# Kernel tuning notes

Hardware: AMD Instinct MI355X
Metric: run time of the kernel (lower is better)

Reference implementation:

```python
import jax, jax.numpy as jnp
import numpy as np

D_MODEL = 1024
N_HEADS = 16
MAX_SEQ_LEN = 2048

def setup_inputs() -> dict:
    key = jax.random.key(0)
    ks = jax.random.split(key, 4)
    B, L, D = 2, 2048, D_MODEL
    s = 0.02
    x = jax.random.normal(ks[0], (B, L, D), dtype=jnp.float32)
    qkv_w = jax.random.normal(ks[1], (D, 3 * D), dtype=jnp.float32) * s
    qkv_b = jnp.zeros((3 * D,), dtype=jnp.float32)
    proj_w = jax.random.normal(ks[2], (D, D), dtype=jnp.float32) * s
    proj_b = jnp.zeros((D,), dtype=jnp.float32)
    bias_table = jax.random.normal(ks[3], (2 * MAX_SEQ_LEN - 1, N_HEADS), dtype=jnp.float32) * s
    return {"x": x, "qkv_w": qkv_w, "qkv_b": qkv_b, "proj_w": proj_w, "proj_b": proj_b, "bias_table": bias_table}

def reference(x, qkv_w, qkv_b, proj_w, proj_b, bias_table):
    B, L, D = x.shape
    H = N_HEADS
    dk = D // H
    scale = dk ** -0.5
    # fused qkv projection: (B,L,3,H,dk)
    qkv = (x @ qkv_w + qkv_b).reshape(B, L, 3, H, dk)
    q = qkv[:, :, 0].transpose(0, 2, 1, 3)  # (B,H,L,dk)
    k = qkv[:, :, 1].transpose(0, 2, 1, 3)
    v = qkv[:, :, 2].transpose(0, 2, 1, 3)
    attn = jnp.einsum("bhqd,bhkd->bhqk", q, k) * scale  # (B,H,L,L)
    # relative position bias gather (Swin-style)
    coords = jnp.arange(L)
    rel_idx = coords[None, :] - coords[:, None] + (MAX_SEQ_LEN - 1)  # (L,L)
    rel_bias = bias_table[rel_idx]  # (L,L,H)
    attn = attn + rel_bias.transpose(2, 0, 1)[None]  # (B,H,L,L)
    attn = jax.nn.softmax(attn, axis=-1)
    out = jnp.einsum("bhqk,bhkd->bhqd", attn, v)  # (B,H,L,dk)
    out = out.transpose(0, 2, 1, 3).reshape(B, L, D)
    return out @ proj_w + proj_b
```

## Files before the change

### kernel.cpp

```cpp
#include <hip/hip_runtime.h>
#include <stdint.h>

typedef __attribute__((ext_vector_type(4))) float    f32x4;
typedef f32x4 __attribute__((aligned(4)))   f32x4u;
typedef __attribute__((ext_vector_type(8))) short    bf16x8;
typedef __attribute__((ext_vector_type(2))) uint32_t u32x2;
typedef __attribute__((ext_vector_type(4))) uint32_t u32x4;

#define MFMA16(a,b,c) __builtin_amdgcn_mfma_f32_16x16x32_bf16((a),(b),(c),0,0,0)

__device__ __forceinline__ uint16_t f2bf(float f){
  uint32_t u = __float_as_uint(f);
  return (uint16_t)((u + 0x7FFFu + ((u >> 16) & 1u)) >> 16);
}

__device__ __forceinline__ uint32_t pk_bf16(float lo, float hi){
  uint32_t r; asm("v_cvt_pk_bf16_f32 %0, %1, %2" : "=v"(r) : "v"(lo), "v"(hi)); return r;
}

__device__ __forceinline__ float fast_exp2(float x){
  float r; asm("v_exp_f32 %0, %1" : "=v"(r) : "v"(x)); return r;
}
__device__ __forceinline__ float fast_log2(float x){
  float r; asm("v_log_f32 %0, %1" : "=v"(r) : "v"(x)); return r;
}

__device__ __forceinline__ float bfl(uint32_t u){ return __uint_as_float(u << 16); }
__device__ __forceinline__ float bfh(uint32_t u){ return __uint_as_float(u & 0xffff0000u); }

__device__ __forceinline__ void gload16(const uint16_t* g, uint16_t* l){
  __builtin_amdgcn_global_load_lds((const __attribute__((address_space(1))) uint32_t*)g,
                                   (__attribute__((address_space(3))) uint32_t*)l, 16, 0, 0);
}

__global__ void k_cvt(const float* __restrict__ in, uint16_t* __restrict__ out){
  const size_t i = (size_t)(blockIdx.x*256 + threadIdx.x) * 4;
  const f32x4 v = *(const f32x4*)(in + i);
  u32x2 pk = {pk_bf16(v[0], v[1]), pk_bf16(v[2], v[3])};
  *(u32x2*)(out + i) = pk;
}

__global__ void k_tcvt(const float* __restrict__ in, uint16_t* __restrict__ out, int K, int N){
  __shared__ float tile[64][65];
  const int k0 = blockIdx.y*64, n0 = blockIdx.x*64;
  const int tc = threadIdx.x & 63, tr = threadIdx.x >> 6;
  #pragma unroll
  for (int p=0;p<16;p++){ int r = p*4 + tr; tile[r][tc] = in[(size_t)(k0+r)*N + n0 + tc]; }
  __syncthreads();
  #pragma unroll
  for (int p=0;p<16;p++){ int r = p*4 + tr; out[(size_t)(n0+r)*K + k0 + tc] = f2bf(tile[tc][r]); }
}

__global__ void k_biast(const float* __restrict__ in, float* __restrict__ out){
  const int i = blockIdx.x*256 + threadIdx.x;
  if (i < 4095*16) out[(i & 15)*4096 + (i >> 4)] = in[i] * 1.4426950408889634f;
}

template<int EPI>
__global__ __launch_bounds__(256, 2) void k_gemm(
    const uint16_t* __restrict__ A, const uint16_t* __restrict__ Bt,
    const float* __restrict__ bias,
    uint16_t* __restrict__ qo, uint16_t* __restrict__ ko, uint16_t* __restrict__ vto,
    float* __restrict__ outf)
{
  __shared__ __align__(16) uint16_t at[128*64];
  __shared__ __align__(16) uint16_t bt[128*64];
  const int tid = threadIdx.x;
  const int lane = tid & 63, w = tid >> 6;
  const int g = lane >> 4, li = lane & 15;
  const int wr = w >> 1, wc = w & 1;
  const int m0 = blockIdx.y * 128, n0 = blockIdx.x * 128;

  f32x4 acc[4][4] = {};

  const int srow = tid >> 3;
  const int scg  = (tid & 7) ^ (srow & 7);

  for (int kt_ = 0; kt_ < 16; kt_++){
    const int kk = kt_*64;
    __syncthreads();
    #pragma unroll
    for (int j = 0; j < 4; j++){
      gload16(A  + (size_t)(m0 + j*32 + srow)*1024 + kk + scg*8, at + (j*256+tid)*8);
      gload16(Bt + (size_t)(n0 + j*32 + srow)*1024 + kk + scg*8, bt + (j*256+tid)*8);
    }
    asm volatile("s_waitcnt vmcnt(0)" ::: "memory");
    __syncthreads();

    bf16x8 af[2][4], bfr[2][4];
    #pragma unroll
    for (int mi=0; mi<4; mi++){
      int row = wr*64 + mi*16 + li, sw = row & 7;
      af[0][mi] = *(const bf16x8*)(at + row*64 + ((g     ^ sw)*8));
      af[1][mi] = *(const bf16x8*)(at + row*64 + (((4+g) ^ sw)*8));
    }
    #pragma unroll
    for (int ni=0; ni<4; ni++){
      int row = wc*64 + ni*16 + li, sw = row & 7;
      bfr[0][ni] = *(const bf16x8*)(bt + row*64 + ((g     ^ sw)*8));
      bfr[1][ni] = *(const bf16x8*)(bt + row*64 + (((4+g) ^ sw)*8));
    }
    #pragma unroll
    for (int s=0; s<2; s++)
      #pragma unroll
      for (int mi=0; mi<4; mi++)
        #pragma unroll
        for (int ni=0; ni<4; ni++)
          acc[mi][ni] = MFMA16(af[s][mi], bfr[s][ni], acc[mi][ni]);
  }

  if (EPI == 0){
    #pragma unroll
    for (int ni=0; ni<4; ni++){
      const int c = n0 + wc*64 + ni*16 + li;
      const float bv = bias[c];
      const int which = c >> 10, cc = c & 1023;
      const int h = cc >> 6, d = cc & 63;
      #pragma unroll
      for (int mi=0; mi<4; mi++){
        const int trow = m0 + wr*64 + mi*16 + g*4;
        const int b_ = trow >> 11, lcl = trow & 2047;
        const f32x4 v4 = acc[mi][ni];
        if (which == 0){
          uint16_t* dst = qo + (((size_t)(b_*16 + h)*2048 + lcl)*64 + d);
          #pragma unroll
          for (int r=0;r<4;r++) dst[(size_t)r*64] = f2bf((v4[r] + bv) * 0.18033688011112042f);
        } else if (which == 1){
          uint16_t* dst = ko + (((size_t)(b_*16 + h)*2048 + lcl)*64 + d);
          #pragma unroll
          for (int r=0;r<4;r++) dst[(size_t)r*64] = f2bf(v4[r] + bv);
        } else {
          u32x2 pk = {pk_bf16(v4[0]+bv, v4[1]+bv), pk_bf16(v4[2]+bv, v4[3]+bv)};
          *(u32x2*)(vto + (((size_t)(b_*16 + h)*64 + d)*2048 + lcl)) = pk;
        }
      }
    }
  } else {
    #pragma unroll
    for (int ni=0; ni<4; ni++){
      const int c = n0 + wc*64 + ni*16 + li;
      const float bv = bias[c];
      #pragma unroll
      for (int mi=0; mi<4; mi++){
        const int trow = m0 + wr*64 + mi*16 + g*4;
        float* dst = outf + (size_t)trow*1024 + c;
        const f32x4 v4 = acc[mi][ni];
        #pragma unroll
        for (int r=0;r<4;r++) dst[(size_t)r*1024] = v4[r] + bv;
      }
    }
  }
}

__device__ __forceinline__ void attn_tile(
    int t, bool last, int tid, int g, int li, int srow, int scg,
    const uint16_t* kbase, const uint16_t* vbase, const float* bb,
    const uint16_t* ktc, uint16_t* ktn, const uint16_t* vtc, uint16_t* vtn, uint16_t* pl,
    const bf16x8 (&qf)[2][2], bf16x8 ones,
    f32x4 (&o)[4][2], f32x4 (&o4)[2], float& mrun0, float& mrun1)
{
  const int kv0 = t*64;

  f32x4 bv[2][4];
  #pragma unroll
  for (int c=0;c<2;c++)
    #pragma unroll
    for (int mf=0;mf<4;mf++)
      bv[c][mf] = *(const f32x4u*)(bb + kv0 + mf*16 + g*4 - c*16 - li);
  asm volatile("" ::: "memory");

  if (!last){
    const int kv1 = kv0 + 64;
    gload16(kbase + (size_t)(kv1+srow)*64 + scg*8,         ktn + tid*8);
    gload16(kbase + (size_t)(kv1+srow+32)*64 + scg*8,      ktn + 2048 + tid*8);
    gload16(vbase + (size_t)srow*2048 + kv1 + scg*8,       vtn + tid*8);
    gload16(vbase + (size_t)(srow+32)*2048 + kv1 + scg*8,  vtn + 2048 + tid*8);
    asm volatile("s_waitcnt vmcnt(12)" ::: "memory");
  } else {
    asm volatile("s_waitcnt vmcnt(8)" ::: "memory");
  }
  __builtin_amdgcn_s_barrier();

  f32x4 sa[4][2];
  __builtin_amdgcn_s_setprio(1);
  #pragma unroll
  for (int mf=0; mf<4; mf++){
    const int row = mf*16 + li, sw = row & 7;
    bf16x8 a0 = *(const bf16x8*)(ktc + row*64 + ((g     ^ sw)*8));
    bf16x8 a1 = *(const bf16x8*)(ktc + row*64 + (((4+g) ^ sw)*8));
    #pragma unroll
    for (int c=0;c<2;c++){
      f32x4 cfr = {};
      cfr = MFMA16(a0, qf[c][0], cfr);
      cfr = MFMA16(a1, qf[c][1], cfr);
      sa[mf][c] = cfr;
    }
  }
  __builtin_amdgcn_s_setprio(0);

  float t0 = -__builtin_inff(), t1 = -__builtin_inff();
  #pragma unroll
  for (int mf=0; mf<4; mf++){
    sa[mf][0] += bv[0][mf];
    sa[mf][1] += bv[1][mf];
    #pragma unroll
    for (int r=0; r<4; r++){
      t0 = fmaxf(t0, sa[mf][0][r]);
      t1 = fmaxf(t1, sa[mf][1][r]);
    }
  }

  const int ok = (t0 <= mrun0 + 8.f) && (t1 <= mrun1 + 8.f);
  if (!__all(ok)){
    float r0 = t0, r1 = t1;
    r0 = fmaxf(r0, __shfl_xor(r0, 16)); r0 = fmaxf(r0, __shfl_xor(r0, 32));
    r1 = fmaxf(r1, __shfl_xor(r1, 16)); r1 = fmaxf(r1, __shfl_xor(r1, 32));
    const float mn0 = fmaxf(mrun0, r0), mn1 = fmaxf(mrun1, r1);
    const float a0 = fast_exp2(mrun0 - mn0), a1 = fast_exp2(mrun1 - mn1);
    #pragma unroll
    for (int mf=0; mf<4; mf++){ o[mf][0] *= a0; o[mf][1] *= a1; }
    o4[0] *= a0; o4[1] *= a1;
    mrun0 = mn0; mrun1 = mn1;
  }

  bf16x8 av[2][4];
  #pragma unroll
  for (int s=0; s<2; s++)
    #pragma unroll
    for (int mf=0; mf<4; mf++){
      const int row = mf*16 + li, sw = row & 7;
      av[s][mf] = *(const bf16x8*)(vtc + row*64 + (((4*s+g) ^ sw)*8));
    }

  const int swp2 = 2*(li & 7);
  #pragma unroll
  for (int c=0;c<2;c++){
    const float mr = c ? mrun1 : mrun0;
    #pragma unroll
    for (int mf=0; mf<4; mf++){
      float p0 = fast_exp2(sa[mf][c][0] - mr);
      float p1 = fast_exp2(sa[mf][c][1] - mr);
      float p2 = fast_exp2(sa[mf][c][2] - mr);
      float p3 = fast_exp2(sa[mf][c][3] - mr);
      u32x2 pk = {pk_bf16(p0,p1), pk_bf16(p2,p3)};
      *(u32x2*)(pl + li*64 + (((4*mf+g) ^ swp2)*4)) = pk;
    }
    __builtin_amdgcn_s_setprio(1);
    #pragma unroll
    for (int s=0; s<2; s++){
      bf16x8 pb = *(const bf16x8*)(pl + li*64 + (((8*s+2*g) ^ swp2)*4));
      o4[c] = MFMA16(ones, pb, o4[c]);
      #pragma unroll
      for (int mf=0; mf<4; mf++)
        o[mf][c] = MFMA16(av[s][mf], pb, o[mf][c]);
    }
    __builtin_amdgcn_s_setprio(0);
  }
  __builtin_amdgcn_s_barrier();
}

__global__ __launch_bounds__(256, 2) void k_attn(
    const uint16_t* __restrict__ qg, const uint16_t* __restrict__ kg,
    const uint16_t* __restrict__ vg, const float* __restrict__ biast,
    uint16_t* __restrict__ opart, float* __restrict__ spart)
{
  __shared__ __align__(16) uint16_t kt[2][64*64];
  __shared__ __align__(16) uint16_t vt[2][64*64];
  __shared__ __align__(16) uint16_t pt[4][16*64];
  const int tid = threadIdx.x;
  const int lane = tid & 63, w = tid >> 6;
  const int g = lane >> 4, li = lane & 15;
  const int bh = blockIdx.y, h = bh & 15, b_ = bh >> 4;
  const int id = blockIdx.x;
  const int split = id & 1, qxi = id >> 1;
  const int qw = qxi*128 + w*32;
  const int tg0 = split*16;

  bf16x8 qf[2][2];
  #pragma unroll
  for (int c=0;c<2;c++){
    const uint16_t* qp = qg + ((size_t)bh*2048 + qw + c*16 + li)*64 + g*8;
    qf[c][0] = *(const bf16x8*)(qp);
    qf[c][1] = *(const bf16x8*)(qp + 32);
  }
  bf16x8 ones = (bf16x8)(short)0;
  if (li == 0){ const short v = (short)0x3F80; ones = (bf16x8){v,v,v,v,v,v,v,v}; }

  f32x4 o[4][2] = {};
  f32x4 o4[2] = {};
  float mrun0 = -__builtin_inff(), mrun1 = -__builtin_inff();

  const uint16_t* kbase = kg + (size_t)bh*(2048*64);
  const uint16_t* vbase = vg + (size_t)bh*(64*2048);
  const int srow = tid >> 3;
  const int scg  = (tid & 7) ^ (srow & 7);
  const float* bb = biast + h*4096 + 2047 - qw;
  uint16_t* pl = &pt[w][0];

  const int kvp = tg0*64;
  gload16(kbase + (size_t)(kvp+srow)*64 + scg*8,        &kt[0][tid*8]);
  gload16(kbase + (size_t)(kvp+srow+32)*64 + scg*8,     &kt[0][2048 + tid*8]);
  gload16(vbase + (size_t)srow*2048 + kvp + scg*8,      &vt[0][tid*8]);
  gload16(vbase + (size_t)(srow+32)*2048 + kvp + scg*8, &vt[0][2048 + tid*8]);

  for (int tt = 0; tt < 16; tt += 2){
    attn_tile(tg0+tt,   false,      tid, g, li, srow, scg, kbase, vbase, bb,
              &kt[0][0], &kt[1][0], &vt[0][0], &vt[1][0], pl,
              qf, ones, o, o4, mrun0, mrun1);
    attn_tile(tg0+tt+1, tt == 14,   tid, g, li, srow, scg, kbase, vbase, bb,
              &kt[1][0], &kt[0][0], &vt[1][0], &vt[0][0], pl,
              qf, ones, o, o4, mrun0, mrun1);
  }

  const float ls0 = __shfl(o4[0][0], li);
  const float ls1 = __shfl(o4[1][0], li);
  const float inv0 = 1.0f / ls0, inv1 = 1.0f / ls1;
  const float sv0 = mrun0 + fast_log2(ls0);
  const float sv1 = mrun1 + fast_log2(ls1);
  #pragma unroll
  for (int c=0;c<2;c++){
    const float inv = c ? inv1 : inv0;
    const int token = b_*2048 + qw + c*16 + li;
    if (g == 0) spart[split*65536 + token*16 + h] = c ? sv1 : sv0;
    uint16_t* dst = opart + ((size_t)(split*4096 + token))*1024 + h*64;
    #pragma unroll
    for (int mf=0; mf<4; mf++){
      u32x2 pk = {pk_bf16(o[mf][c][0]*inv, o[mf][c][1]*inv),
                  pk_bf16(o[mf][c][2]*inv, o[mf][c][3]*inv)};
      *(u32x2*)(dst + mf*16 + g*4) = pk;
    }
  }
}

__global__ void k_merge(const uint16_t* __restrict__ op, const float* __restrict__ sp,
                        uint16_t* __restrict__ ao){
  const int gid = blockIdx.x*256 + threadIdx.x;
  const int token = gid >> 7, col0 = (gid & 127) * 8, h = col0 >> 6;
  const float s0 = sp[token*16 + h], s1 = sp[65536 + token*16 + h];
  const float sm = fmaxf(s0, s1);
  float w0 = fast_exp2(s0 - sm), w1 = fast_exp2(s1 - sm);
  const float inv = 1.0f / (w0 + w1);
  w0 *= inv; w1 *= inv;
  const size_t i0 = (size_t)token*1024 + col0;
  const u32x4 a = *(const u32x4*)(op + i0);
  const u32x4 b = *(const u32x4*)(op + (size_t)4096*1024 + i0);
  u32x4 r;
  #pragma unroll
  for (int j=0;j<4;j++){
    const float e0 = w0*bfl(a[j]) + w1*bfl(b[j]);
    const float e1 = w0*bfh(a[j]) + w1*bfh(b[j]);
    r[j] = pk_bf16(e0, e1);
  }
  *(u32x4*)(ao + i0) = r;
}

extern "C" void kernel_launch(void* const* d_in, const int* in_sizes, int n_in,
                              void* d_out, int out_size, void* d_ws, size_t ws_size,
                              hipStream_t stream)
{
  const float* x      = (const float*)d_in[0];
  const float* qkv_w  = (const float*)d_in[1];
  const float* qkv_b  = (const float*)d_in[2];
  const float* proj_w = (const float*)d_in[3];
  const float* proj_b = (const float*)d_in[4];
  const float* btab   = (const float*)d_in[5];
  float* out = (float*)d_out;

  char* p = (char*)d_ws;
  uint16_t* x_bf    = (uint16_t*)(p);
  uint16_t* qkv_wt  = (uint16_t*)(p + 8388608);
  uint16_t* proj_wt = (uint16_t*)(p + 14680064);
  uint16_t* q_buf   = (uint16_t*)(p + 16777216);
  uint16_t* k_buf   = (uint16_t*)(p + 25165824);
  uint16_t* vt_buf  = (uint16_t*)(p + 33554432);
  uint16_t* ao_buf  = (uint16_t*)(p + 41943040);
  float*    bias_t  = (float*)   (p + 50331648);

  uint16_t* o_part = (uint16_t*)d_out;
  float*    s_part = (float*)p;

  k_cvt  <<<dim3(4096),  dim3(256), 0, stream>>>(x, x_bf);
  k_tcvt <<<dim3(48,16), dim3(256), 0, stream>>>(qkv_w,  qkv_wt,  1024, 3072);
  k_tcvt <<<dim3(16,16), dim3(256), 0, stream>>>(proj_w, proj_wt, 1024, 1024);
  k_biast<<<dim3(256),   dim3(256), 0, stream>>>(btab, bias_t);

  k_gemm<0><<<dim3(24,32), dim3(256), 0, stream>>>(x_bf, qkv_wt, qkv_b, q_buf, k_buf, vt_buf, nullptr);
  k_attn   <<<dim3(32,32), dim3(256), 0, stream>>>(q_buf, k_buf, vt_buf, bias_t, o_part, s_part);
  k_merge  <<<dim3(2048),  dim3(256), 0, stream>>>(o_part, s_part, ao_buf);
  k_gemm<1><<<dim3(8,32),  dim3(256), 0, stream>>>(ao_buf, proj_wt, proj_b, nullptr, nullptr, nullptr, out);
}
```

Baseline: 131.0 us.

## Fuse bias-table prep into cvt kernel, narrow proj GEMM tile, dedupe bias loads

Merges the bias-table transpose into the x conversion kernel, removing one launch. Splits the output projection into its own GEMM with 128x64 tiles, doubling its grid from 256 to 512 blocks so more CUs are busy. In the attention tile, the 8 overlapping bias vector loads become 5 shared loads, and the vmcnt waits are adjusted to match. The trade-off is more blocks with less reuse per block in the projection GEMM.

```diff
diff --git a/kernel.cpp b/kernel.cpp
--- a/kernel.cpp
+++ b/kernel.cpp
@@ -33,11 +33,18 @@
                                    (__attribute__((address_space(3))) uint32_t*)l, 16, 0, 0);
 }
 
-__global__ void k_cvt(const float* __restrict__ in, uint16_t* __restrict__ out){
-  const size_t i = (size_t)(blockIdx.x*256 + threadIdx.x) * 4;
-  const f32x4 v = *(const f32x4*)(in + i);
-  u32x2 pk = {pk_bf16(v[0], v[1]), pk_bf16(v[2], v[3])};
-  *(u32x2*)(out + i) = pk;
+__global__ void k_cvtb(const float* __restrict__ in, uint16_t* __restrict__ out,
+                       const float* __restrict__ btab, float* __restrict__ bias_t){
+  const int bx = blockIdx.x;
+  if (bx < 4096){
+    const size_t i = (size_t)(bx*256 + threadIdx.x) * 4;
+    const f32x4 v = *(const f32x4*)(in + i);
+    u32x2 pk = {pk_bf16(v[0], v[1]), pk_bf16(v[2], v[3])};
+    *(u32x2*)(out + i) = pk;
+  } else {
+    const int i = (bx - 4096)*256 + threadIdx.x;
+    if (i < 4095*16) bias_t[(i & 15)*4096 + (i >> 4)] = btab[i] * 1.4426950408889634f;
+  }
 }
 
 __global__ void k_tcvt(const float* __restrict__ in, uint16_t* __restrict__ out, int K, int N){
@@ -51,17 +58,10 @@
   for (int p=0;p<16;p++){ int r = p*4 + tr; out[(size_t)(n0+r)*K + k0 + tc] = f2bf(tile[tc][r]); }
 }
 
-__global__ void k_biast(const float* __restrict__ in, float* __restrict__ out){
-  const int i = blockIdx.x*256 + threadIdx.x;
-  if (i < 4095*16) out[(i & 15)*4096 + (i >> 4)] = in[i] * 1.4426950408889634f;
-}
-
-template<int EPI>
 __global__ __launch_bounds__(256, 2) void k_gemm(
     const uint16_t* __restrict__ A, const uint16_t* __restrict__ Bt,
     const float* __restrict__ bias,
-    uint16_t* __restrict__ qo, uint16_t* __restrict__ ko, uint16_t* __restrict__ vto,
-    float* __restrict__ outf)
+    uint16_t* __restrict__ qo, uint16_t* __restrict__ ko, uint16_t* __restrict__ vto)
 {
   __shared__ __align__(16) uint16_t at[128*64];
   __shared__ __align__(16) uint16_t bt[128*64];
@@ -109,45 +109,94 @@
           acc[mi][ni] = MFMA16(af[s][mi], bfr[s][ni], acc[mi][ni]);
   }
 
-  if (EPI == 0){
-    #pragma unroll
-    for (int ni=0; ni<4; ni++){
-      const int c = n0 + wc*64 + ni*16 + li;
-      const float bv = bias[c];
-      const int which = c >> 10, cc = c & 1023;
-      const int h = cc >> 6, d = cc & 63;
+  #pragma unroll
+  for (int ni=0; ni<4; ni++){
+    const int c = n0 + wc*64 + ni*16 + li;
+    const float bv = bias[c];
+    const int which = c >> 10, cc = c & 1023;
+    const int h = cc >> 6, d = cc & 63;
+    #pragma unroll
+    for (int mi=0; mi<4; mi++){
+      const int trow = m0 + wr*64 + mi*16 + g*4;
+      const int b_ = trow >> 11, lcl = trow & 2047;
+      const f32x4 v4 = acc[mi][ni];
+      if (which == 0){
+        uint16_t* dst = qo + (((size_t)(b_*16 + h)*2048 + lcl)*64 + d);
+        #pragma unroll
+        for (int r=0;r<4;r++) dst[(size_t)r*64] = f2bf((v4[r] + bv) * 0.18033688011112042f);
+      } else if (which == 1){
+        uint16_t* dst = ko + (((size_t)(b_*16 + h)*2048 + lcl)*64 + d);
+        #pragma unroll
+        for (int r=0;r<4;r++) dst[(size_t)r*64] = f2bf(v4[r] + bv);
+      } else {
+        u32x2 pk = {pk_bf16(v4[0]+bv, v4[1]+bv), pk_bf16(v4[2]+bv, v4[3]+bv)};
+        *(u32x2*)(vto + (((size_t)(b_*16 + h)*64 + d)*2048 + lcl)) = pk;
+      }
+    }
+  }
+}
+
+__global__ __launch_bounds__(256, 2) void k_gemm2(
+    const uint16_t* __restrict__ A, const uint16_t* __restrict__ Bt,
+    const float* __restrict__ bias, float* __restrict__ outf)
+{
+  __shared__ __align__(16) uint16_t at[128*64];
+  __shared__ __align__(16) uint16_t bt[64*64];
+  const int tid = threadIdx.x;
+  const int lane = tid & 63, w = tid >> 6;
+  const int g = lane >> 4, li = lane & 15;
+  const int wr = w >> 1, wc = w & 1;
+  const int m0 = blockIdx.y * 128, n0 = blockIdx.x * 64;
+
+  f32x4 acc[4][2] = {};
+  const int srow = tid >> 3;
+  const int scg  = (tid & 7) ^ (srow & 7);
+
+  for (int kt_ = 0; kt_ < 16; kt_++){
+    const int kk = kt_*64;
+    __syncthreads();
+    #pragma unroll
+    for (int j = 0; j < 4; j++)
+      gload16(A  + (size_t)(m0 + j*32 + srow)*1024 + kk + scg*8, at + (j*256+tid)*8);
+    #pragma unroll
+    for (int j = 0; j < 2; j++)
+      gload16(Bt + (size_t)(n0 + j*32 + srow)*1024 + kk + scg*8, bt + (j*256+tid)*8);
+    asm volatile("s_waitcnt vmcnt(0)" ::: "memory");
+    __syncthreads();
+
+    bf16x8 af[2][4], bfr[2][2];
+    #pragma unroll
+    for (int mi=0; mi<4; mi++){
+      int row = wr*64 + mi*16 + li, sw = row & 7;
+      af[0][mi] = *(const bf16x8*)(at + row*64 + ((g     ^ sw)*8));
+      af[1][mi] = *(const bf16x8*)(at + row*64 + (((4+g) ^ sw)*8));
+    }
+    #pragma unroll
+    for (int ni=0; ni<2; ni++){
+      int row = wc*32 + ni*16 + li, sw = row & 7;
+      bfr[0][ni] = *(const bf16x8*)(bt + row*64 + ((g     ^ sw)*8));
+      bfr[1][ni] = *(const bf16x8*)(bt + row*64 + (((4+g) ^ sw)*8));
+    }
+    #pragma unroll
+    for (int s=0; s<2; s++)
       #pragma unroll
-      for (int mi=0; mi<4; mi++){
-        const int trow = m0 + wr*64 + mi*16 + g*4;
-        const int b_ = trow >> 11, lcl = trow & 2047;
-        const f32x4 v4 = acc[mi][ni];
-        if (which == 0){
-          uint16_t* dst = qo + (((size_t)(b_*16 + h)*2048 + lcl)*64 + d);
-          #pragma unroll
-          for (int r=0;r<4;r++) dst[(size_t)r*64] = f2bf((v4[r] + bv) * 0.18033688011112042f);
-        } else if (which == 1){
-          uint16_t* dst = ko + (((size_t)(b_*16 + h)*2048 + lcl)*64 + d);
-          #pragma unroll
-          for (int r=0;r<4;r++) dst[(size_t)r*64] = f2bf(v4[r] + bv);
-        } else {
-          u32x2 pk = {pk_bf16(v4[0]+bv, v4[1]+bv), pk_bf16(v4[2]+bv, v4[3]+bv)};
-          *(u32x2*)(vto + (((size_t)(b_*16 + h)*64 + d)*2048 + lcl)) = pk;
-        }
-      }
-    }
-  } else {
-    #pragma unroll
-    for (int ni=0; ni<4; ni++){
-      const int c = n0 + wc*64 + ni*16 + li;
-      const float bv = bias[c];
+      for (int mi=0; mi<4; mi++)
+        #pragma unroll
+        for (int ni=0; ni<2; ni++)
+          acc[mi][ni] = MFMA16(af[s][mi], bfr[s][ni], acc[mi][ni]);
+  }
+
+  #pragma unroll
+  for (int ni=0; ni<2; ni++){
+    const int c = n0 + wc*32 + ni*16 + li;
+    const float bv = bias[c];
+    #pragma unroll
+    for (int mi=0; mi<4; mi++){
+      const int trow = m0 + wr*64 + mi*16 + g*4;
+      float* dst = outf + (size_t)trow*1024 + c;
+      const f32x4 v4 = acc[mi][ni];
       #pragma unroll
-      for (int mi=0; mi<4; mi++){
-        const int trow = m0 + wr*64 + mi*16 + g*4;
-        float* dst = outf + (size_t)trow*1024 + c;
-        const f32x4 v4 = acc[mi][ni];
-        #pragma unroll
-        for (int r=0;r<4;r++) dst[(size_t)r*1024] = v4[r] + bv;
-      }
+      for (int r=0;r<4;r++) dst[(size_t)r*1024] = v4[r] + bv;
     }
   }
 }
@@ -161,12 +210,10 @@
 {
   const int kv0 = t*64;
 
-  f32x4 bv[2][4];
-  #pragma unroll
-  for (int c=0;c<2;c++)
-    #pragma unroll
-    for (int mf=0;mf<4;mf++)
-      bv[c][mf] = *(const f32x4u*)(bb + kv0 + mf*16 + g*4 - c*16 - li);
+  f32x4 bv5[5];
+  #pragma unroll
+  for (int j=0;j<5;j++)
+    bv5[j] = *(const f32x4u*)(bb + kv0 + (j-1)*16 + g*4 - li);
   asm volatile("" ::: "memory");
 
   if (!last){
@@ -175,9 +222,9 @@
     gload16(kbase + (size_t)(kv1+srow+32)*64 + scg*8,      ktn + 2048 + tid*8);
     gload16(vbase + (size_t)srow*2048 + kv1 + scg*8,       vtn + tid*8);
     gload16(vbase + (size_t)(srow+32)*2048 + kv1 + scg*8,  vtn + 2048 + tid*8);
-    asm volatile("s_waitcnt vmcnt(12)" ::: "memory");
+    asm volatile("s_waitcnt vmcnt(9)" ::: "memory");
   } else {
-    asm volatile("s_waitcnt vmcnt(8)" ::: "memory");
+    asm volatile("s_waitcnt vmcnt(5)" ::: "memory");
   }
   __builtin_amdgcn_s_barrier();
 
@@ -201,8 +248,8 @@
   float t0 = -__builtin_inff(), t1 = -__builtin_inff();
   #pragma unroll
   for (int mf=0; mf<4; mf++){
-    sa[mf][0] += bv[0][mf];
-    sa[mf][1] += bv[1][mf];
+    sa[mf][0] += bv5[mf+1];
+    sa[mf][1] += bv5[mf];
     #pragma unroll
     for (int r=0; r<4; r++){
       t0 = fmaxf(t0, sa[mf][0][r]);
@@ -379,13 +426,12 @@
   uint16_t* o_part = (uint16_t*)d_out;
   float*    s_part = (float*)p;
 
-  k_cvt  <<<dim3(4096),  dim3(256), 0, stream>>>(x, x_bf);
+  k_cvtb <<<dim3(4352),  dim3(256), 0, stream>>>(x, x_bf, btab, bias_t);
   k_tcvt <<<dim3(48,16), dim3(256), 0, stream>>>(qkv_w,  qkv_wt,  1024, 3072);
   k_tcvt <<<dim3(16,16), dim3(256), 0, stream>>>(proj_w, proj_wt, 1024, 1024);
-  k_biast<<<dim3(256),   dim3(256), 0, stream>>>(btab, bias_t);
-
-  k_gemm<0><<<dim3(24,32), dim3(256), 0, stream>>>(x_bf, qkv_wt, qkv_b, q_buf, k_buf, vt_buf, nullptr);
+
+  k_gemm   <<<dim3(24,32), dim3(256), 0, stream>>>(x_bf, qkv_wt, qkv_b, q_buf, k_buf, vt_buf);
   k_attn   <<<dim3(32,32), dim3(256), 0, stream>>>(q_buf, k_buf, vt_buf, bias_t, o_part, s_part);
   k_merge  <<<dim3(2048),  dim3(256), 0, stream>>>(o_part, s_part, ao_buf);
-  k_gemm<1><<<dim3(8,32),  dim3(256), 0, stream>>>(ao_buf, proj_wt, proj_b, nullptr, nullptr, nullptr, out);
-}
+  k_gemm2  <<<dim3(16,32), dim3(256), 0, stream>>>(ao_buf, proj_wt, proj_b, out);
+}
```

Result: faster. 124.4 us (-5.0%).
